# Kernel optimization log

Hardware: AMD Instinct MI355X
Metric: run time of the kernel (lower is better)

## Reference

```python
import jax, jax.numpy as jnp
import numpy as np

TEMP = 0.5  # matches init_kwargs temperature


def setup_inputs() -> dict:
    key = jax.random.key(0)
    k1, k2 = jax.random.split(key)
    B, D = 4096, 256
    return {
        "z_i": jax.random.normal(k1, (B, D), dtype=jnp.float32),
        "z_j": jax.random.normal(k2, (B, D), dtype=jnp.float32),
    }


def reference(z_i, z_j):
    B = z_i.shape[0]
    N = 2 * B
    z = jnp.concatenate([z_i, z_j], axis=0)          # [N, D]
    sim = (z @ z.T) / TEMP                            # [N, N]

    # Faithful to source: BOTH positive halves come from diag(sim, +B)
    pos = jnp.concatenate([jnp.diagonal(sim, offset=B)] * 2)  # [N]

    # Arithmetic mask: exclude diagonal and the +/-B off-diagonals (static)
    idx = np.arange(N)
    mask = (idx[:, None] != idx[None, :]) & (np.abs(idx[:, None] - idx[None, :]) != B)
    neg = jnp.where(jnp.asarray(mask), sim, -jnp.inf)          # [N, N]

    # logits = [pos | negatives], label = 0 -> CE_i = lse(logits_i) - pos_i
    logits = jnp.concatenate([pos[:, None], neg], axis=1)      # [N, N+1]
    lse = jax.nn.logsumexp(logits, axis=1)                     # [N]
    loss = jnp.mean(lse - pos) / N                             # CE mean, then /N as in source
    return loss
```

## Files before the change

### kernel.cpp

```cpp
#include <hip/hip_runtime.h>
#include <hip/hip_bf16.h>

#define DD 256
#define NN 8192
#define B_ROWS 4096
#define NRG 64
#define NCJ 128
#define NBLK 4160
#define M_FIX 160.0f
#define SCALE 1.6986436f
#define LN2 0.69314718055994531f

typedef __attribute__((ext_vector_type(8))) short bf16x8;
typedef __attribute__((ext_vector_type(4))) float f32x4;

__device__ __forceinline__ unsigned short f2bf(float f) {
    unsigned int x = __float_as_uint(f);
    x += 0x7fffu + ((x >> 16) & 1u);
    return (unsigned short)(x >> 16);
}
__device__ __forceinline__ float bf2f(unsigned short u) {
    return __uint_as_float((unsigned int)u << 16);
}
__device__ __forceinline__ float exp2_raw(float x) {
    float r; asm("v_exp_f32 %0, %1" : "=v"(r) : "v"(x)); return r;
}
__device__ __forceinline__ void gload16(const unsigned short* g, unsigned short* l) {
    __builtin_amdgcn_global_load_lds(
        (const __attribute__((address_space(1))) void*)g,
        (__attribute__((address_space(3))) void*)l, 16, 0, 0);
}

__global__ void cast_pos_kernel(const float* __restrict__ zi, const float* __restrict__ zj,
                                unsigned short* __restrict__ zb, float* __restrict__ pos) {
    const int w = threadIdx.x >> 6;
    const int l = threadIdx.x & 63;
    const int r = blockIdx.x * 4 + w;
    const float4 a = ((const float4*)(zi + (size_t)r * DD))[l];
    const float4 b = ((const float4*)(zj + (size_t)r * DD))[l];
    float d = a.x * b.x + a.y * b.y + a.z * b.z + a.w * b.w;
    #pragma unroll
    for (int off = 32; off > 0; off >>= 1) d += __shfl_down(d, off, 64);
    if (l == 0) pos[r] = 2.0f * d;
    ushort4 oa, ob;
    oa.x = f2bf(a.x * SCALE); oa.y = f2bf(a.y * SCALE);
    oa.z = f2bf(a.z * SCALE); oa.w = f2bf(a.w * SCALE);
    ob.x = f2bf(b.x * SCALE); ob.y = f2bf(b.y * SCALE);
    ob.z = f2bf(b.z * SCALE); ob.w = f2bf(b.w * SCALE);
    ((ushort4*)(zb + (size_t)r * DD))[l] = oa;
    ((ushort4*)(zb + (size_t)(r + B_ROWS) * DD))[l] = ob;
}

__global__ __launch_bounds__(256, 4) void simlse_kernel(const unsigned short* __restrict__ zb,
                                                        unsigned short* __restrict__ PT) {
    __shared__ unsigned short tile[32 * 512];
    const int tid = threadIdx.x;
    const int w  = tid >> 6;
    const int l  = tid & 63;
    const int lg = l >> 4;
    const int lr = l & 15;

    const int wg = ((int)blockIdx.x & 7) * (NBLK / 8) + ((int)blockIdx.x >> 3);
    int b = wg, rg = 0;
    while (b >= NCJ - 2 * rg) { b -= NCJ - 2 * rg; ++rg; }
    const int cj = 2 * rg + b;
    const bool mirror = (cj >= 2 * rg + 2);
    const int rbase = rg * 128 + w * 32;
    const int cbase = cj * 64;
    const int ri_u0 = rg * 8 + w * 2;

    #pragma unroll
    for (int jj = 0; jj < 8; ++jj)
        gload16(zb + (size_t)(cbase + w * 16 + lr) * DD + jj * 32 + lg * 8,
                tile + (w * 8 + jj) * 512);

    bf16x8 aF[2][8];
    #pragma unroll
    for (int rt = 0; rt < 2; ++rt) {
        const unsigned short* ap = zb + (size_t)(rbase + rt * 16 + lr) * DD + lg * 8;
        #pragma unroll
        for (int ks = 0; ks < 8; ++ks) aF[rt][ks] = *(const bf16x8*)(ap + ks * 32);
    }

    float rs[2][4];
    #pragma unroll
    for (int rt = 0; rt < 2; ++rt)
        #pragma unroll
        for (int j = 0; j < 4; ++j) rs[rt][j] = 0.f;
    float cs[4];
    #pragma unroll
    for (int sl = 0; sl < 4; ++sl) cs[sl] = 0.f;

    __syncthreads();

    #pragma unroll
    for (int sl = 0; sl < 4; ++sl) {
        f32x4 acc[2];
        acc[0] = (f32x4){0.f, 0.f, 0.f, 0.f};
        acc[1] = (f32x4){0.f, 0.f, 0.f, 0.f};
        #pragma unroll
        for (int ks = 0; ks < 8; ++ks) {
            bf16x8 bF = *(const bf16x8*)(tile + (sl * 8 + ks) * 512 + l * 8);
            acc[0] = __builtin_amdgcn_mfma_f32_16x16x32_bf16(aF[0][ks], bF, acc[0], 0, 0, 0);
            acc[1] = __builtin_amdgcn_mfma_f32_16x16x32_bf16(aF[1][ks], bF, acc[1], 0, 0, 0);
        }
        const int ci_u = cj * 4 + sl;
        #pragma unroll
        for (int rt = 0; rt < 2; ++rt) {
            const bool dt = (!mirror) && (ri_u0 + rt == ci_u);
            #pragma unroll
            for (int j = 0; j < 4; ++j) {
                float e = exp2_raw(acc[rt][j] - M_FIX);
                if (dt && (lr == lg * 4 + j)) e = 0.f;
                rs[rt][j] += e;
                cs[sl] += e;
            }
        }
    }

    #pragma unroll
    for (int rt = 0; rt < 2; ++rt)
        #pragma unroll
        for (int j = 0; j < 4; ++j) {
            float v = rs[rt][j];
            v += __shfl_xor(v, 1, 64);
            v += __shfl_xor(v, 2, 64);
            v += __shfl_xor(v, 4, 64);
            v += __shfl_xor(v, 8, 64);
            rs[rt][j] = v;
        }
    if (lr == 0) {
        #pragma unroll
        for (int rt = 0; rt < 2; ++rt)
            #pragma unroll
            for (int j = 0; j < 4; ++j)
                PT[(size_t)cj * NN + rbase + rt * 16 + lg * 4 + j] = f2bf(rs[rt][j]);
    }

    if (mirror) {
        #pragma unroll
        for (int sl = 0; sl < 4; ++sl) {
            float v = cs[sl];
            v += __shfl_xor(v, 16, 64);
            v += __shfl_xor(v, 32, 64);
            cs[sl] = v;
        }
        __syncthreads();
        float* red = (float*)tile;
        if (lg == 0) {
            #pragma unroll
            for (int sl = 0; sl < 4; ++sl) red[w * 64 + sl * 16 + lr] = cs[sl];
        }
        __syncthreads();
        if (tid < 64) {
            const float v = red[tid] + red[64 + tid] + red[128 + tid] + red[192 + tid];
            PT[(size_t)(2 * rg) * NN + cbase + tid] = f2bf(v);
        }
    }
}

__global__ __launch_bounds__(128) void rowmerge_kernel(const unsigned short* __restrict__ PT,
                                                       const float* __restrict__ pos,
                                                       float* __restrict__ partial) {
    const int r = blockIdx.x * 128 + threadIdx.x;
    const int rg = r >> 7;
    float S = 0.f;
    #pragma unroll
    for (int s = 0; s < NCJ; ++s) {
        const float v = bf2f(PT[(size_t)s * NN + r]);
        const bool valid = (s >= 2 * rg) || ((s & 1) == 0);
        S += valid ? v : 0.f;
    }
    float val = M_FIX * LN2 + logf(S);
    if (r < B_ROWS) val -= 2.0f * pos[r];
    __shared__ float red[128];
    red[threadIdx.x] = val;
    __syncthreads();
    for (int st = 64; st > 0; st >>= 1) {
        if (threadIdx.x < st) red[threadIdx.x] += red[threadIdx.x + st];
        __syncthreads();
    }
    if (threadIdx.x == 0) partial[blockIdx.x] = red[0];
}

__global__ void final_kernel(const float* __restrict__ partial, float* __restrict__ out) {
    float v = partial[threadIdx.x];
    #pragma unroll
    for (int off = 32; off > 0; off >>= 1) v += __shfl_down(v, off, 64);
    if (threadIdx.x == 0) out[0] = v / (8192.f * 8192.f);
}

extern "C" void kernel_launch(void* const* d_in, const int* in_sizes, int n_in,
                              void* d_out, int out_size, void* d_ws, size_t ws_size,
                              hipStream_t stream) {
    const float* zi = (const float*)d_in[0];
    const float* zj = (const float*)d_in[1];
    float* out = (float*)d_out;
    char* ws = (char*)d_ws;

    unsigned short* zb = (unsigned short*)ws;
    unsigned short* PT = (unsigned short*)(ws + (size_t)NN * DD * 2);
    float* pos     = (float*)(ws + (size_t)NN * DD * 2 + (size_t)NCJ * NN * 2);
    float* partial = pos + B_ROWS;

    hipLaunchKernelGGL(cast_pos_kernel, dim3(B_ROWS / 4), dim3(256), 0, stream, zi, zj, zb, pos);
    hipLaunchKernelGGL(simlse_kernel,   dim3(NBLK), dim3(256), 0, stream, zb, PT);
    hipLaunchKernelGGL(rowmerge_kernel, dim3(NN / 128), dim3(128), 0, stream, PT, pos, partial);
    hipLaunchKernelGGL(final_kernel,    dim3(1), dim3(64), 0, stream, partial, out);
}
```

Measured before the change: 67.47 us.

## Split simlse work across 8 waves and parallelize rowmerge column reduction

The similarity/LSE kernel now uses 512 threads per block, with each of 8 waves handling one 16-row tile instead of two. The tile load and the cross-wave column reduction are redistributed to match. The row-merge kernel splits each row's 128-slice sum across 8 threads with shuffle reduction, using 256 blocks instead of 64, and the final kernel reduces 256 partials. The intent is more waves in flight to hide latency and a wider reduction stage, at the cost of larger blocks, lower MFMA reuse per wave and more LDS reduction traffic.

```diff
diff --git a/kernel.cpp b/kernel.cpp
--- a/kernel.cpp
+++ b/kernel.cpp
@@ -51,7 +51,7 @@
     ((ushort4*)(zb + (size_t)(r + B_ROWS) * DD))[l] = ob;
 }
 
-__global__ __launch_bounds__(256, 4) void simlse_kernel(const unsigned short* __restrict__ zb,
+__global__ __launch_bounds__(512, 8) void simlse_kernel(const unsigned short* __restrict__ zb,
                                                         unsigned short* __restrict__ PT) {
     __shared__ unsigned short tile[32 * 512];
     const int tid = threadIdx.x;
@@ -65,76 +65,60 @@
     while (b >= NCJ - 2 * rg) { b -= NCJ - 2 * rg; ++rg; }
     const int cj = 2 * rg + b;
     const bool mirror = (cj >= 2 * rg + 2);
-    const int rbase = rg * 128 + w * 32;
+    const int rbase = rg * 128 + w * 16;
     const int cbase = cj * 64;
-    const int ri_u0 = rg * 8 + w * 2;
-
-    #pragma unroll
-    for (int jj = 0; jj < 8; ++jj)
-        gload16(zb + (size_t)(cbase + w * 16 + lr) * DD + jj * 32 + lg * 8,
-                tile + (w * 8 + jj) * 512);
-
-    bf16x8 aF[2][8];
-    #pragma unroll
-    for (int rt = 0; rt < 2; ++rt) {
-        const unsigned short* ap = zb + (size_t)(rbase + rt * 16 + lr) * DD + lg * 8;
-        #pragma unroll
-        for (int ks = 0; ks < 8; ++ks) aF[rt][ks] = *(const bf16x8*)(ap + ks * 32);
-    }
-
-    float rs[2][4];
-    #pragma unroll
-    for (int rt = 0; rt < 2; ++rt)
-        #pragma unroll
-        for (int j = 0; j < 4; ++j) rs[rt][j] = 0.f;
-    float cs[4];
-    #pragma unroll
-    for (int sl = 0; sl < 4; ++sl) cs[sl] = 0.f;
+    const int ri_u  = rg * 8 + w;
+
+    #pragma unroll
+    for (int jj = 0; jj < 4; ++jj) {
+        const int slot = w * 4 + jj, sl = slot >> 3, ks = slot & 7;
+        gload16(zb + (size_t)(cbase + sl * 16 + lr) * DD + ks * 32 + lg * 8,
+                tile + slot * 512);
+    }
+
+    bf16x8 aF[8];
+    {
+        const unsigned short* ap = zb + (size_t)(rbase + lr) * DD + lg * 8;
+        #pragma unroll
+        for (int ks = 0; ks < 8; ++ks) aF[ks] = *(const bf16x8*)(ap + ks * 32);
+    }
+
+    float rs[4] = {0.f, 0.f, 0.f, 0.f};
+    float cs[4] = {0.f, 0.f, 0.f, 0.f};
 
     __syncthreads();
 
     #pragma unroll
     for (int sl = 0; sl < 4; ++sl) {
-        f32x4 acc[2];
-        acc[0] = (f32x4){0.f, 0.f, 0.f, 0.f};
-        acc[1] = (f32x4){0.f, 0.f, 0.f, 0.f};
+        f32x4 acc = (f32x4){0.f, 0.f, 0.f, 0.f};
         #pragma unroll
         for (int ks = 0; ks < 8; ++ks) {
             bf16x8 bF = *(const bf16x8*)(tile + (sl * 8 + ks) * 512 + l * 8);
-            acc[0] = __builtin_amdgcn_mfma_f32_16x16x32_bf16(aF[0][ks], bF, acc[0], 0, 0, 0);
-            acc[1] = __builtin_amdgcn_mfma_f32_16x16x32_bf16(aF[1][ks], bF, acc[1], 0, 0, 0);
-        }
-        const int ci_u = cj * 4 + sl;
-        #pragma unroll
-        for (int rt = 0; rt < 2; ++rt) {
-            const bool dt = (!mirror) && (ri_u0 + rt == ci_u);
-            #pragma unroll
-            for (int j = 0; j < 4; ++j) {
-                float e = exp2_raw(acc[rt][j] - M_FIX);
-                if (dt && (lr == lg * 4 + j)) e = 0.f;
-                rs[rt][j] += e;
-                cs[sl] += e;
-            }
-        }
-    }
-
-    #pragma unroll
-    for (int rt = 0; rt < 2; ++rt)
+            acc = __builtin_amdgcn_mfma_f32_16x16x32_bf16(aF[ks], bF, acc, 0, 0, 0);
+        }
+        const bool dt = (!mirror) && (ri_u == cj * 4 + sl);
         #pragma unroll
         for (int j = 0; j < 4; ++j) {
-            float v = rs[rt][j];
-            v += __shfl_xor(v, 1, 64);
-            v += __shfl_xor(v, 2, 64);
-            v += __shfl_xor(v, 4, 64);
-            v += __shfl_xor(v, 8, 64);
-            rs[rt][j] = v;
-        }
+            float e = exp2_raw(acc[j] - M_FIX);
+            if (dt && (lr == lg * 4 + j)) e = 0.f;
+            rs[j] += e;
+            cs[sl] += e;
+        }
+    }
+
+    #pragma unroll
+    for (int j = 0; j < 4; ++j) {
+        float v = rs[j];
+        v += __shfl_xor(v, 1, 64);
+        v += __shfl_xor(v, 2, 64);
+        v += __shfl_xor(v, 4, 64);
+        v += __shfl_xor(v, 8, 64);
+        rs[j] = v;
+    }
     if (lr == 0) {
         #pragma unroll
-        for (int rt = 0; rt < 2; ++rt)
-            #pragma unroll
-            for (int j = 0; j < 4; ++j)
-                PT[(size_t)cj * NN + rbase + rt * 16 + lg * 4 + j] = f2bf(rs[rt][j]);
+        for (int j = 0; j < 4; ++j)
+            PT[(size_t)cj * NN + rbase + lg * 4 + j] = f2bf(rs[j]);
     }
 
     if (mirror) {
@@ -153,41 +137,61 @@
         }
         __syncthreads();
         if (tid < 64) {
-            const float v = red[tid] + red[64 + tid] + red[128 + tid] + red[192 + tid];
+            float v = 0.f;
+            #pragma unroll
+            for (int ww = 0; ww < 8; ++ww) v += red[ww * 64 + tid];
             PT[(size_t)(2 * rg) * NN + cbase + tid] = f2bf(v);
         }
     }
 }
 
-__global__ __launch_bounds__(128) void rowmerge_kernel(const unsigned short* __restrict__ PT,
+__global__ __launch_bounds__(256) void rowmerge_kernel(const unsigned short* __restrict__ PT,
                                                        const float* __restrict__ pos,
                                                        float* __restrict__ partial) {
-    const int r = blockIdx.x * 128 + threadIdx.x;
+    const int tid = threadIdx.x;
+    const int rloc = tid >> 3;
+    const int sg   = tid & 7;
+    const int r  = blockIdx.x * 32 + rloc;
     const int rg = r >> 7;
     float S = 0.f;
     #pragma unroll
-    for (int s = 0; s < NCJ; ++s) {
+    for (int k = 0; k < 16; ++k) {
+        const int s = sg * 16 + k;
         const float v = bf2f(PT[(size_t)s * NN + r]);
         const bool valid = (s >= 2 * rg) || ((s & 1) == 0);
         S += valid ? v : 0.f;
     }
-    float val = M_FIX * LN2 + logf(S);
-    if (r < B_ROWS) val -= 2.0f * pos[r];
-    __shared__ float red[128];
-    red[threadIdx.x] = val;
+    S += __shfl_xor(S, 1, 64);
+    S += __shfl_xor(S, 2, 64);
+    S += __shfl_xor(S, 4, 64);
+    __shared__ float red[32];
+    if (sg == 0) {
+        float val = M_FIX * LN2 + logf(S);
+        if (r < B_ROWS) val -= 2.0f * pos[r];
+        red[rloc] = val;
+    }
     __syncthreads();
-    for (int st = 64; st > 0; st >>= 1) {
-        if (threadIdx.x < st) red[threadIdx.x] += red[threadIdx.x + st];
-        __syncthreads();
-    }
-    if (threadIdx.x == 0) partial[blockIdx.x] = red[0];
-}
-
-__global__ void final_kernel(const float* __restrict__ partial, float* __restrict__ out) {
-    float v = partial[threadIdx.x];
+    if (tid < 32) {
+        float v = red[tid];
+        v += __shfl_xor(v, 1, 64);
+        v += __shfl_xor(v, 2, 64);
+        v += __shfl_xor(v, 4, 64);
+        v += __shfl_xor(v, 8, 64);
+        v += __shfl_xor(v, 16, 64);
+        if (tid == 0) partial[blockIdx.x] = v;
+    }
+}
+
+__global__ __launch_bounds__(256) void final_kernel(const float* __restrict__ partial,
+                                                    float* __restrict__ out) {
+    const int tid = threadIdx.x;
+    float v = partial[tid];
     #pragma unroll
     for (int off = 32; off > 0; off >>= 1) v += __shfl_down(v, off, 64);
-    if (threadIdx.x == 0) out[0] = v / (8192.f * 8192.f);
+    __shared__ float red[4];
+    if ((tid & 63) == 0) red[tid >> 6] = v;
+    __syncthreads();
+    if (tid == 0) out[0] = (red[0] + red[1] + red[2] + red[3]) / (8192.f * 8192.f);
 }
 
 extern "C" void kernel_launch(void* const* d_in, const int* in_sizes, int n_in,
@@ -204,7 +208,7 @@
     float* partial = pos + B_ROWS;
 
     hipLaunchKernelGGL(cast_pos_kernel, dim3(B_ROWS / 4), dim3(256), 0, stream, zi, zj, zb, pos);
-    hipLaunchKernelGGL(simlse_kernel,   dim3(NBLK), dim3(256), 0, stream, zb, PT);
-    hipLaunchKernelGGL(rowmerge_kernel, dim3(NN / 128), dim3(128), 0, stream, PT, pos, partial);
-    hipLaunchKernelGGL(final_kernel,    dim3(1), dim3(64), 0, stream, partial, out);
-}
+    hipLaunchKernelGGL(simlse_kernel,   dim3(NBLK), dim3(512), 0, stream, zb, PT);
+    hipLaunchKernelGGL(rowmerge_kernel, dim3(NN / 32), dim3(256), 0, stream, PT, pos, partial);
+    hipLaunchKernelGGL(final_kernel,    dim3(1), dim3(256), 0, stream, partial, out);
+}
```

Result: faster. 65.20 us (-3.4%).
